# Optimization experiments

Hardware: AMD Instinct MI355X
Metric: run time of the kernel (lower is better)

The kernel has to match this reference:

```python
import jax, jax.numpy as jnp
import numpy as np

HEADS = 2
NEG_SLOPE = 0.2
B, T, N, F_IN = 4, 8, 10000, 128
HID = 128
E = 320000
OUT = 10


def setup_inputs() -> dict:
    key = jax.random.key(0)
    ks = jax.random.split(key, 16)
    d = {}
    d['x_seq'] = jax.random.normal(ks[0], (B, T, N, F_IN), dtype=jnp.float32)
    d['edge_index'] = jax.random.randint(ks[1], (T, 2, E), 0, N)
    def glorot(k, shape):
        fan = shape[0]
        return jax.random.normal(k, shape, dtype=jnp.float32) / jnp.sqrt(jnp.float32(fan))
    # GAT layer 1: in=F_IN, heads=2, out per head=HID
    d['W1'] = glorot(ks[2], (F_IN, HEADS * HID))
    d['a_src1'] = jax.random.normal(ks[3], (HEADS, HID), dtype=jnp.float32) * 0.1
    d['a_dst1'] = jax.random.normal(ks[4], (HEADS, HID), dtype=jnp.float32) * 0.1
    d['b1'] = jnp.zeros((HEADS * HID,), jnp.float32)
    # GAT layer 2: in=2*HID
    d['W2'] = glorot(ks[5], (HEADS * HID, HEADS * HID))
    d['a_src2'] = jax.random.normal(ks[6], (HEADS, HID), dtype=jnp.float32) * 0.1
    d['a_dst2'] = jax.random.normal(ks[7], (HEADS, HID), dtype=jnp.float32) * 0.1
    d['b2'] = jnp.zeros((HEADS * HID,), jnp.float32)
    # GRU: input 2*HID, hidden HID (torch layout: [3H, in])
    d['Wih'] = glorot(ks[8], (3 * HID, HEADS * HID)) 
    d['Whh'] = glorot(ks[9], (3 * HID, HID))
    d['bih'] = jnp.zeros((3 * HID,), jnp.float32)
    d['bhh'] = jnp.zeros((3 * HID,), jnp.float32)
    # classifier
    d['Wc'] = glorot(ks[10], (HID, OUT))
    d['bc'] = jnp.zeros((OUT,), jnp.float32)
    return d


def _gat_layer(x, src, dst, W, a_s, a_d, b):
    # x: [N, Fin]; src/dst: [E'] (self-loops included)
    n = x.shape[0]
    dh = a_s.shape[1]
    h = (x @ W).reshape(n, HEADS, dh)                    # [N, H, dh]
    es = jnp.einsum('nhd,hd->nh', h, a_s)                # [N, H]
    ed = jnp.einsum('nhd,hd->nh', h, a_d)
    e = jax.nn.leaky_relu(es[src] + ed[dst], NEG_SLOPE)  # [E', H]
    m = jax.ops.segment_max(e, dst, num_segments=n)      # stable softmax per dst
    ex = jnp.exp(e - m[dst])
    denom = jax.ops.segment_sum(ex, dst, num_segments=n)
    alpha = ex / denom[dst]                              # [E', H]
    out = jax.ops.segment_sum(h[src] * alpha[:, :, None], dst, num_segments=n)
    return out.reshape(n, HEADS * dh) + b


def _gru(seq, Wih, Whh, bih, bhh):
    # seq: [B, T, D] -> outputs [B, T, H]
    b, t, _ = seq.shape
    hdim = Whh.shape[1]
    def step(hprev, x):
        gi = x @ Wih.T + bih
        gh = hprev @ Whh.T + bhh
        i_r, i_z, i_n = jnp.split(gi, 3, axis=-1)
        h_r, h_z, h_n = jnp.split(gh, 3, axis=-1)
        r = jax.nn.sigmoid(i_r + h_r)
        z = jax.nn.sigmoid(i_z + h_z)
        nn_ = jnp.tanh(i_n + r * h_n)
        hnew = (1.0 - z) * nn_ + z * hprev
        return hnew, hnew
    h0 = jnp.zeros((b, hdim), seq.dtype)
    _, ys = jax.lax.scan(step, h0, jnp.swapaxes(seq, 0, 1))
    return jnp.swapaxes(ys, 0, 1)


def reference(x_seq, edge_index, W1, a_src1, a_dst1, b1, W2, a_src2, a_dst2, b2,
              Wih, Whh, bih, bhh, Wc, bc):
    n = x_seq.shape[2]
    loops = jnp.arange(n)
    # add self-loops per timestep (PyG GATConv default)
    src = jnp.concatenate([edge_index[:, 0], jnp.broadcast_to(loops, (edge_index.shape[0], n))], axis=1)
    dst = jnp.concatenate([edge_index[:, 1], jnp.broadcast_to(loops, (edge_index.shape[0], n))], axis=1)

    def block(x, s, d):
        x1 = jax.nn.relu(_gat_layer(x, s, d, W1, a_src1, a_dst1, b1))
        x2 = _gat_layer(x1, s, d, W2, a_src2, a_dst2, b2)
        return x2.mean(axis=0)                          # node mean-pool -> [2*HID]

    per_t = jax.vmap(lambda xt, s, d: jax.vmap(lambda xb: block(xb, s, d))(xt))
    # x_seq [B,T,N,F] -> [T,B,N,F]
    pooled = per_t(jnp.swapaxes(x_seq, 0, 1), src, dst)  # [T, B, 2*HID]
    seq = jnp.swapaxes(pooled, 0, 1)                     # [B, T, 2*HID]

    rnn_out = _gru(seq, Wih, Whh, bih, bhh)              # [B, T, HID]
    final = rnn_out.mean(axis=1)                         # dropout p=0 is identity
    return final @ Wc + bc
```

## Files before the change

kernel.cpp:

```cpp
#include <hip/hip_runtime.h>
#include <cstdint>

#define NB 4
#define TT 8
#define NN 10000
#define FIN 128
#define HID 128
#define EE 320000
#define DMODEL 256
#define MTOT (NB*NN)
#define NEG 0.2f

__device__ __forceinline__ float leaky(float x){ return x >= 0.f ? x : NEG*x; }

__global__ void hist_kernel(const int* __restrict__ eidx, int* __restrict__ counts){
  int idx = blockIdx.x*256 + threadIdx.x;
  int t = idx / EE, e = idx - t*EE;
  int dst = eidx[(size_t)t*2*EE + EE + e];
  atomicAdd(&counts[t*NN + dst], 1);
}

__global__ void scan_kernel(const int* __restrict__ counts, int* __restrict__ rp,
                            int* __restrict__ cursor){
  int t = blockIdx.x; int tid = threadIdx.x;
  __shared__ int lds[256];
  const int CH = 40;
  int lo = tid*CH, hi = lo+CH < NN ? lo+CH : NN;
  int s = 0;
  for (int i = lo; i < hi; ++i) s += counts[t*NN + i];
  lds[tid] = s; __syncthreads();
  for (int off = 1; off < 256; off <<= 1){
    int v = (tid >= off) ? lds[tid-off] : 0; __syncthreads();
    lds[tid] += v; __syncthreads();
  }
  int run = (tid == 0) ? 0 : lds[tid-1];
  for (int i = lo; i < hi; ++i){
    rp[t*(NN+1) + i] = run; cursor[t*NN + i] = run; run += counts[t*NN + i];
  }
  if (tid == 255) rp[t*(NN+1) + NN] = lds[255];
}

__global__ void scatter_kernel(const int* __restrict__ eidx, int* __restrict__ cursor,
                               int* __restrict__ ssrc){
  int idx = blockIdx.x*256 + threadIdx.x;
  int t = idx / EE, e = idx - t*EE;
  int src = eidx[(size_t)t*2*EE + e];
  int dst = eidx[(size_t)t*2*EE + EE + e];
  int pos = atomicAdd(&cursor[t*NN + dst], 1);
  ssrc[(size_t)t*EE + pos] = src;
}

template<int K>
__global__ __launch_bounds__(256) void gemm_attn_kernel(const float* __restrict__ A0,
    const float* __restrict__ A1, size_t bstride,
    const float* __restrict__ W, const float* __restrict__ av_s, const float* __restrict__ av_d,
    float* __restrict__ C, float* __restrict__ es, float* __restrict__ ed, int M){
  __shared__ float As[16][132];
  __shared__ float Bs[16][128];
  int tid = threadIdx.x;
  int r0 = blockIdx.x*128, c0 = blockIdx.y*128;
  int ty = tid >> 4, tx = tid & 15;

  int cq = (tid & 3)*4;
  const float* a0r0; const float* a0r1; const float* a1r0 = nullptr; const float* a1r1 = nullptr;
  {
    int r_ = r0 + (tid >> 2); if (r_ >= M) r_ = M-1;
    int b = r_/NN, n = r_ - b*NN;
    a0r0 = A0 + (size_t)b*bstride + (size_t)n*128 + cq;
    if (K > 128) a1r0 = A1 + (size_t)r_*128 + cq;
    r_ = r0 + 64 + (tid >> 2); if (r_ >= M) r_ = M-1;
    b = r_/NN; n = r_ - b*NN;
    a0r1 = A0 + (size_t)b*bstride + (size_t)n*128 + cq;
    if (K > 128) a1r1 = A1 + (size_t)r_*128 + cq;
  }
  const float* brow0 = W + (size_t)(tid>>5)*DMODEL + c0 + (tid & 31)*4;
  const float* brow1 = W + (size_t)((tid>>5)+8)*DMODEL + c0 + (tid & 31)*4;

  float acc[8][8];
  #pragma unroll
  for (int i = 0; i < 8; ++i)
    #pragma unroll
    for (int j = 0; j < 8; ++j) acc[i][j] = 0.f;

  int r_loc = tid >> 2;
  #pragma unroll 1
  for (int half = 0; half < K/128; ++half){
    const float* pr0 = half ? a1r0 : a0r0;
    const float* pr1 = half ? a1r1 : a0r1;
    #pragma unroll 1
    for (int k0 = 0; k0 < 128; k0 += 16){
      int kab = half*128 + k0;
      float4 a0v = *(const float4*)(pr0 + k0);
      float4 a1v = *(const float4*)(pr1 + k0);
      float4 b0v = *(const float4*)(brow0 + (size_t)kab*DMODEL);
      float4 b1v = *(const float4*)(brow1 + (size_t)kab*DMODEL);
      __syncthreads();
      As[cq+0][r_loc] = a0v.x; As[cq+1][r_loc] = a0v.y; As[cq+2][r_loc] = a0v.z; As[cq+3][r_loc] = a0v.w;
      As[cq+0][64+r_loc] = a1v.x; As[cq+1][64+r_loc] = a1v.y; As[cq+2][64+r_loc] = a1v.z; As[cq+3][64+r_loc] = a1v.w;
      *(float4*)&Bs[tid>>5][(tid&31)*4]     = b0v;
      *(float4*)&Bs[(tid>>5)+8][(tid&31)*4] = b1v;
      __syncthreads();
      #pragma unroll
      for (int kk = 0; kk < 16; ++kk){
        float4 aA = *(const float4*)&As[kk][ty*4];
        float4 aB = *(const float4*)&As[kk][64+ty*4];
        float4 bA = *(const float4*)&Bs[kk][tx*4];
        float4 bB = *(const float4*)&Bs[kk][64+tx*4];
        float ar[8] = {aA.x,aA.y,aA.z,aA.w,aB.x,aB.y,aB.z,aB.w};
        float br[8] = {bA.x,bA.y,bA.z,bA.w,bB.x,bB.y,bB.z,bB.w};
        #pragma unroll
        for (int i = 0; i < 8; ++i)
          #pragma unroll
          for (int j = 0; j < 8; ++j) acc[i][j] += ar[i]*br[j];
      }
    }
  }

  float as_c[8], ad_c[8];
  #pragma unroll
  for (int j = 0; j < 8; ++j){
    int c = c0 + (j < 4 ? tx*4+j : 64+tx*4+(j-4));
    as_c[j] = av_s[c]; ad_c[j] = av_d[c];
  }
  int hsel = c0 >> 7;
  float* Ch = C + (size_t)hsel*M*128;
  #pragma unroll
  for (int ii = 0; ii < 8; ++ii){
    int r = r0 + (ii < 4 ? ty*4+ii : 64+ty*4+(ii-4));
    float ls = 0.f, ld_ = 0.f;
    #pragma unroll
    for (int j = 0; j < 8; ++j){ ls += acc[ii][j]*as_c[j]; ld_ += acc[ii][j]*ad_c[j]; }
    #pragma unroll
    for (int o = 8; o > 0; o >>= 1){ ls += __shfl_down(ls, o); ld_ += __shfl_down(ld_, o); }
    if (r < M){
      if (tx == 0){ es[(size_t)hsel*M + r] = ls; ed[(size_t)hsel*M + r] = ld_; }
      *(float4*)&Ch[(size_t)r*128 + tx*4]      = make_float4(acc[ii][0],acc[ii][1],acc[ii][2],acc[ii][3]);
      *(float4*)&Ch[(size_t)r*128 + 64 + tx*4] = make_float4(acc[ii][4],acc[ii][5],acc[ii][6],acc[ii][7]);
    }
  }
}

__global__ __launch_bounds__(128) void agg_kernel(const float* __restrict__ H,
    const float* __restrict__ es, const float* __restrict__ ed,
    const int* __restrict__ rp, const int* __restrict__ ssrc,
    const float* __restrict__ bias, float* __restrict__ out, int do_relu){
  int d = blockIdx.x; int ph = blockIdx.y;
  int h = ph & 1, b = ph >> 1;
  int tid = threadIdx.x;
  const size_t reg = (size_t)h*MTOT + (size_t)b*NN;
  const float* esh = es + reg;
  const float* edh = ed + reg;
  const float* Hh  = H + reg*128;
  int e0 = rp[d], e1 = rp[d+1];
  __shared__ float sred[2];
  __shared__ float sbc2[2];
  __shared__ unsigned int offs[128];
  __shared__ float lal[128];

  float edv  = edh[d];
  float self = leaky(esh[d] + edv);

  float m = self;
  for (int e = e0 + tid; e < e1; e += 128) m = fmaxf(m, leaky(esh[ssrc[e]] + edv));
  #pragma unroll
  for (int o = 32; o > 0; o >>= 1) m = fmaxf(m, __shfl_down(m, o));
  int w = tid >> 6, lane = tid & 63;
  if (lane == 0) sred[w] = m;
  __syncthreads();
  if (tid == 0) sbc2[0] = fmaxf(sred[0], sred[1]);
  __syncthreads();
  m = sbc2[0];

  float s0 = (tid == 0) ? expf(self - m) : 0.f;
  for (int e = e0 + tid; e < e1; e += 128) s0 += expf(leaky(esh[ssrc[e]] + edv) - m);
  #pragma unroll
  for (int o = 32; o > 0; o >>= 1) s0 += __shfl_down(s0, o);
  if (lane == 0) sred[w] = s0;
  __syncthreads();
  if (tid == 0) sbc2[1] = 1.f/(sred[0] + sred[1]);
  __syncthreads();
  float inv = sbc2[1];

  float acc = expf(self - m) * inv * Hh[(size_t)d*128 + tid];
  const char* Hb = (const char*)Hh + (size_t)tid*4;
  for (int ch = e0; ch < e1; ch += 128){
    int nc = (e1 - ch < 128) ? (e1 - ch) : 128;
    __syncthreads();
    if (tid < nc){
      int s = ssrc[ch + tid];
      offs[tid] = (unsigned int)(s*512);
      lal[tid]  = expf(leaky(esh[s] + edv) - m) * inv;
    }
    __syncthreads();
    int i = 0;
    float a0 = 0.f, a1 = 0.f, a2 = 0.f, a3 = 0.f;
    for (; i + 4 <= nc; i += 4){
      a0 += lal[i+0] * *(const float*)(Hb + offs[i+0]);
      a1 += lal[i+1] * *(const float*)(Hb + offs[i+1]);
      a2 += lal[i+2] * *(const float*)(Hb + offs[i+2]);
      a3 += lal[i+3] * *(const float*)(Hb + offs[i+3]);
    }
    for (; i < nc; ++i) a0 += lal[i] * *(const float*)(Hb + offs[i]);
    acc += (a0 + a1) + (a2 + a3);
  }
  acc += bias[h*128 + tid];
  if (do_relu) acc = fmaxf(acc, 0.f);
  out[(reg + d)*128 + tid] = acc;
}

#define PCH 64
__global__ void pool1_kernel(const float* __restrict__ X2, float* __restrict__ part){
  int b = blockIdx.x / PCH; int ch = blockIdx.x % PCH; int c = threadIdx.x;
  const int RPC = (NN + PCH - 1) / PCH;
  int d0 = ch*RPC, d1 = d0+RPC < NN ? d0+RPC : NN;
  int hreg = c >> 7, cw = c & 127;
  const float* Xr = X2 + ((size_t)hreg*MTOT + (size_t)b*NN)*128 + cw;
  float s = 0.f;
  for (int d = d0; d < d1; ++d) s += Xr[(size_t)d*128];
  part[(size_t)blockIdx.x*DMODEL + c] = s;
}
__global__ void pool2_kernel(const float* __restrict__ part, float* __restrict__ pooled, int t){
  int b = blockIdx.x; int c = threadIdx.x;
  float s = 0.f;
  for (int ch = 0; ch < PCH; ++ch) s += part[(size_t)(b*PCH + ch)*DMODEL + c];
  pooled[(size_t)(t*NB + b)*DMODEL + c] = s * (1.f/NN);
}

__global__ __launch_bounds__(384) void gi_kernel(const float* __restrict__ pooled,
    const float* __restrict__ Wih, const float* __restrict__ bih, float* __restrict__ gi){
  int row = blockIdx.x; int j = threadIdx.x;
  __shared__ float xs[256];
  if (j < 256) xs[j] = pooled[(size_t)row*DMODEL + j];
  __syncthreads();
  const float4* Wr = (const float4*)(Wih + (size_t)j*DMODEL);
  float s = bih[j];
  #pragma unroll 8
  for (int k = 0; k < 64; ++k){
    float4 wv = Wr[k];
    s += wv.x*xs[k*4] + wv.y*xs[k*4+1] + wv.z*xs[k*4+2] + wv.w*xs[k*4+3];
  }
  gi[(size_t)row*384 + j] = s;
}

__global__ __launch_bounds__(384) void rec_kernel(const float* __restrict__ gi,
    const float* __restrict__ Whh, const float* __restrict__ bhh,
    const float* __restrict__ Wc, const float* __restrict__ bc, float* __restrict__ outp){
  int b = blockIdx.x; int j = threadIdx.x;
  __shared__ float hs[128], ghs[384], fin[128];
  if (j < 128) hs[j] = 0.f;
  float macc = 0.f;
  const float4* Ur = (const float4*)(Whh + (size_t)j*HID);
  float bh = bhh[j];
  for (int t = 0; t < TT; ++t){
    __syncthreads();
    float s = bh;
    #pragma unroll 8
    for (int k = 0; k < 32; ++k){
      float4 wv = Ur[k];
      s += wv.x*hs[k*4] + wv.y*hs[k*4+1] + wv.z*hs[k*4+2] + wv.w*hs[k*4+3];
    }
    ghs[j] = s; __syncthreads();
    float hnew = 0.f;
    if (j < 128){
      const float* g = gi + (size_t)(t*NB + b)*384;
      float r = 1.f/(1.f + expf(-(g[j] + ghs[j])));
      float z = 1.f/(1.f + expf(-(g[128+j] + ghs[128+j])));
      float n = tanhf(g[256+j] + r*ghs[256+j]);
      hnew = (1.f - z)*n + z*hs[j];
    }
    __syncthreads();
    if (j < 128){ hs[j] = hnew; macc += hnew; }
  }
  if (j < 128) fin[j] = macc * (1.f/TT);
  __syncthreads();
  if (j < 10){
    float s = bc[j];
    for (int k = 0; k < 128; ++k) s += fin[k]*Wc[k*10 + j];
    outp[b*10 + j] = s;
  }
}

extern "C" void kernel_launch(void* const* d_in, const int* in_sizes, int n_in,
                              void* d_out, int out_size, void* d_ws, size_t ws_size,
                              hipStream_t stream){
  const float* x_seq = (const float*)d_in[0];
  const int*   eidx  = (const int*)d_in[1];
  const float* W1    = (const float*)d_in[2];
  const float* a_s1  = (const float*)d_in[3];
  const float* a_d1  = (const float*)d_in[4];
  const float* b1    = (const float*)d_in[5];
  const float* W2    = (const float*)d_in[6];
  const float* a_s2  = (const float*)d_in[7];
  const float* a_d2  = (const float*)d_in[8];
  const float* b2    = (const float*)d_in[9];
  const float* Wih   = (const float*)d_in[10];
  const float* Whh   = (const float*)d_in[11];
  const float* bih   = (const float*)d_in[12];
  const float* bhh   = (const float*)d_in[13];
  const float* Wc    = (const float*)d_in[14];
  const float* bc    = (const float*)d_in[15];
  float* outp = (float*)d_out;

  char* ws = (char*)d_ws;
  size_t off = 0;
  auto alloc = [&](size_t bytes)->char*{
    char* p = ws + off; off += (bytes + 511) & ~(size_t)511; return p;
  };
  int*   counts = (int*)  alloc((size_t)TT*NN*4);
  int*   rp     = (int*)  alloc((size_t)TT*(NN+1)*4);
  int*   cursor = (int*)  alloc((size_t)TT*NN*4);
  int*   ssrc   = (int*)  alloc((size_t)TT*EE*4);
  float* H      = (float*)alloc((size_t)MTOT*DMODEL*4);
  float* X1     = (float*)alloc((size_t)MTOT*DMODEL*4);
  float* es     = (float*)alloc((size_t)2*MTOT*4);
  float* ed     = (float*)alloc((size_t)2*MTOT*4);
  float* part   = (float*)alloc((size_t)NB*PCH*DMODEL*4);
  float* pooled = (float*)alloc((size_t)TT*NB*DMODEL*4);
  float* gib    = (float*)alloc((size_t)TT*NB*384*4);
  (void)ws_size; (void)in_sizes; (void)n_in; (void)out_size;

  const int M = MTOT;
  const int GX = (M + 127)/128;

  hipMemsetAsync(counts, 0, (size_t)TT*NN*4, stream);
  hist_kernel   <<<(TT*EE)/256, 256, 0, stream>>>(eidx, counts);
  scan_kernel   <<<TT, 256, 0, stream>>>(counts, rp, cursor);
  scatter_kernel<<<(TT*EE)/256, 256, 0, stream>>>(eidx, cursor, ssrc);

  for (int t = 0; t < TT; ++t){
    const int* rpt = rp + t*(NN+1);
    const int* st  = ssrc + (size_t)t*EE;
    gemm_attn_kernel<FIN><<<dim3(GX, 2), 256, 0, stream>>>(
        x_seq + (size_t)t*NN*FIN, nullptr, (size_t)TT*NN*FIN, W1, a_s1, a_d1, H, es, ed, M);
    agg_kernel<<<dim3(NN, NB*2), 128, 0, stream>>>(H, es, ed, rpt, st, b1, X1, 1);
    gemm_attn_kernel<DMODEL><<<dim3(GX, 2), 256, 0, stream>>>(
        X1, X1 + (size_t)M*128, (size_t)NN*128, W2, a_s2, a_d2, H, es, ed, M);
    agg_kernel<<<dim3(NN, NB*2), 128, 0, stream>>>(H, es, ed, rpt, st, b2, X1, 0);
    pool1_kernel<<<NB*PCH, 256, 0, stream>>>(X1, part);
    pool2_kernel<<<NB, 256, 0, stream>>>(part, pooled, t);
  }
  gi_kernel <<<TT*NB, 384, 0, stream>>>(pooled, Wih, bih, gib);
  rec_kernel<<<NB, 384, 0, stream>>>(gib, Whh, bhh, Wc, bc, outp);
}
```

Baseline: 4.213 ms.

## Use online softmax in GAT aggregation and interleave batch/head blocks per node

Result: faster. 3.894 ms (-7.6%).

```diff
diff --git a/kernel.cpp b/kernel.cpp
--- a/kernel.cpp
+++ b/kernel.cpp
@@ -144,7 +144,9 @@
     const float* __restrict__ es, const float* __restrict__ ed,
     const int* __restrict__ rp, const int* __restrict__ ssrc,
     const float* __restrict__ bias, float* __restrict__ out, int do_relu){
-  int d = blockIdx.x; int ph = blockIdx.y;
+  int bid = blockIdx.x;
+  int ph = bid & 7;
+  int d  = bid >> 3;
   int h = ph & 1, b = ph >> 1;
   int tid = threadIdx.x;
   const size_t reg = (size_t)h*MTOT + (size_t)b*NN;
@@ -152,33 +154,43 @@
   const float* edh = ed + reg;
   const float* Hh  = H + reg*128;
   int e0 = rp[d], e1 = rp[d+1];
-  __shared__ float sred[2];
+  __shared__ float smm[2], sss[2];
   __shared__ float sbc2[2];
+  __shared__ float vcache[128];
   __shared__ unsigned int offs[128];
   __shared__ float lal[128];
 
   float edv  = edh[d];
   float self = leaky(esh[d] + edv);
 
-  float m = self;
-  for (int e = e0 + tid; e < e1; e += 128) m = fmaxf(m, leaky(esh[ssrc[e]] + edv));
+  float m = -1e30f, ssum = 0.f;
+  for (int e = e0 + tid; e < e1; e += 128){
+    int s = ssrc[e];
+    float v = leaky(esh[s] + edv);
+    if (e - e0 < 128){ vcache[tid] = v; offs[tid] = (unsigned int)(s*512); }
+    float mn = fmaxf(m, v);
+    ssum = ssum*expf(m - mn) + expf(v - mn);
+    m = mn;
+  }
   #pragma unroll
-  for (int o = 32; o > 0; o >>= 1) m = fmaxf(m, __shfl_down(m, o));
+  for (int o = 32; o > 0; o >>= 1){
+    float m2 = __shfl_down(m, o);
+    float s2 = __shfl_down(ssum, o);
+    float mn = fmaxf(m, m2);
+    ssum = ssum*expf(m - mn) + s2*expf(m2 - mn);
+    m = mn;
+  }
   int w = tid >> 6, lane = tid & 63;
-  if (lane == 0) sred[w] = m;
+  if (lane == 0){ smm[w] = m; sss[w] = ssum; }
   __syncthreads();
-  if (tid == 0) sbc2[0] = fmaxf(sred[0], sred[1]);
+  if (tid == 0){
+    float mA = smm[0], sA = sss[0], mB = smm[1], sB = sss[1];
+    float mn = fmaxf(fmaxf(mA, mB), self);
+    float st = sA*expf(mA - mn) + sB*expf(mB - mn) + expf(self - mn);
+    sbc2[0] = mn; sbc2[1] = 1.f/st;
+  }
   __syncthreads();
   m = sbc2[0];
-
-  float s0 = (tid == 0) ? expf(self - m) : 0.f;
-  for (int e = e0 + tid; e < e1; e += 128) s0 += expf(leaky(esh[ssrc[e]] + edv) - m);
-  #pragma unroll
-  for (int o = 32; o > 0; o >>= 1) s0 += __shfl_down(s0, o);
-  if (lane == 0) sred[w] = s0;
-  __syncthreads();
-  if (tid == 0) sbc2[1] = 1.f/(sred[0] + sred[1]);
-  __syncthreads();
   float inv = sbc2[1];
 
   float acc = expf(self - m) * inv * Hh[(size_t)d*128 + tid];
@@ -187,9 +199,13 @@
     int nc = (e1 - ch < 128) ? (e1 - ch) : 128;
     __syncthreads();
     if (tid < nc){
-      int s = ssrc[ch + tid];
-      offs[tid] = (unsigned int)(s*512);
-      lal[tid]  = expf(leaky(esh[s] + edv) - m) * inv;
+      if (ch == e0){
+        lal[tid] = expf(vcache[tid] - m) * inv;
+      } else {
+        int s = ssrc[ch + tid];
+        offs[tid] = (unsigned int)(s*512);
+        lal[tid]  = expf(leaky(esh[s] + edv) - m) * inv;
+      }
     }
     __syncthreads();
     int i = 0;
@@ -332,10 +348,10 @@
     const int* st  = ssrc + (size_t)t*EE;
     gemm_attn_kernel<FIN><<<dim3(GX, 2), 256, 0, stream>>>(
         x_seq + (size_t)t*NN*FIN, nullptr, (size_t)TT*NN*FIN, W1, a_s1, a_d1, H, es, ed, M);
-    agg_kernel<<<dim3(NN, NB*2), 128, 0, stream>>>(H, es, ed, rpt, st, b1, X1, 1);
+    agg_kernel<<<8*NN, 128, 0, stream>>>(H, es, ed, rpt, st, b1, X1, 1);
     gemm_attn_kernel<DMODEL><<<dim3(GX, 2), 256, 0, stream>>>(
         X1, X1 + (size_t)M*128, (size_t)NN*128, W2, a_s2, a_d2, H, es, ed, M);
-    agg_kernel<<<dim3(NN, NB*2), 128, 0, stream>>>(H, es, ed, rpt, st, b2, X1, 0);
+    agg_kernel<<<8*NN, 128, 0, stream>>>(H, es, ed, rpt, st, b2, X1, 0);
     pool1_kernel<<<NB*PCH, 256, 0, stream>>>(X1, part);
     pool2_kernel<<<NB, 256, 0, stream>>>(part, pooled, t);
   }
```

## Restructure GAT aggregation: cache first-chunk logits, float4 gathers, interleave batch/head blocks

Applied to the files above, without the earlier changes.

Measured after the change: 3.393 ms. 19.5% less time.

```diff
diff --git a/kernel.cpp b/kernel.cpp
--- a/kernel.cpp
+++ b/kernel.cpp
@@ -144,7 +144,9 @@
     const float* __restrict__ es, const float* __restrict__ ed,
     const int* __restrict__ rp, const int* __restrict__ ssrc,
     const float* __restrict__ bias, float* __restrict__ out, int do_relu){
-  int d = blockIdx.x; int ph = blockIdx.y;
+  int bid = blockIdx.x;
+  int ph = bid & 7;
+  int d  = bid >> 3;
   int h = ph & 1, b = ph >> 1;
   int tid = threadIdx.x;
   const size_t reg = (size_t)h*MTOT + (size_t)b*NN;
@@ -152,60 +154,99 @@
   const float* edh = ed + reg;
   const float* Hh  = H + reg*128;
   int e0 = rp[d], e1 = rp[d+1];
+  int deg = e1 - e0;
+  int nc0 = deg < 128 ? deg : 128;
   __shared__ float sred[2];
   __shared__ float sbc2[2];
-  __shared__ unsigned int offs[128];
-  __shared__ float lal[128];
+  __shared__ float vcache[128];
+  __shared__ unsigned int offsc[128];
+  __shared__ float2 lalf2[128];
+  __shared__ float4 sacc[128];
 
   float edv  = edh[d];
   float self = leaky(esh[d] + edv);
+  int w = tid >> 6, lane = tid & 63;
 
   float m = self;
-  for (int e = e0 + tid; e < e1; e += 128) m = fmaxf(m, leaky(esh[ssrc[e]] + edv));
+  for (int e = e0 + tid; e < e1; e += 128){
+    int s = ssrc[e];
+    float v = leaky(esh[s] + edv);
+    if (e - e0 < 128){ vcache[tid] = v; offsc[tid] = (unsigned int)(s*512); }
+    m = fmaxf(m, v);
+  }
   #pragma unroll
   for (int o = 32; o > 0; o >>= 1) m = fmaxf(m, __shfl_down(m, o));
-  int w = tid >> 6, lane = tid & 63;
   if (lane == 0) sred[w] = m;
   __syncthreads();
   if (tid == 0) sbc2[0] = fmaxf(sred[0], sred[1]);
   __syncthreads();
   m = sbc2[0];
 
-  float s0 = (tid == 0) ? expf(self - m) : 0.f;
-  for (int e = e0 + tid; e < e1; e += 128) s0 += expf(leaky(esh[ssrc[e]] + edv) - m);
-  #pragma unroll
-  for (int o = 32; o > 0; o >>= 1) s0 += __shfl_down(s0, o);
-  if (lane == 0) sred[w] = s0;
-  __syncthreads();
-  if (tid == 0) sbc2[1] = 1.f/(sred[0] + sred[1]);
+  float p = 0.f;
+  if (tid < nc0) p = expf(vcache[tid] - m);
+  float ssum = p;
+  for (int e = e0 + 128 + tid; e < e1; e += 128)
+    ssum += expf(leaky(esh[ssrc[e]] + edv) - m);
+  #pragma unroll
+  for (int o = 32; o > 0; o >>= 1) ssum += __shfl_down(ssum, o);
+  if (lane == 0) sred[w] = ssum;
+  __syncthreads();
+  if (tid == 0) sbc2[1] = 1.f/(sred[0] + sred[1] + expf(self - m));
   __syncthreads();
   float inv = sbc2[1];
-
-  float acc = expf(self - m) * inv * Hh[(size_t)d*128 + tid];
-  const char* Hb = (const char*)Hh + (size_t)tid*4;
+  if (tid < nc0) lalf2[tid] = make_float2(p*inv, __uint_as_float(offsc[tid]));
+  __syncthreads();
+
+  int q = tid >> 5, c = tid & 31;
+  const char* Hbase = (const char*)Hh;
+  unsigned cb = (unsigned)(c*16);
+  float4 accA = make_float4(0.f,0.f,0.f,0.f);
+  float4 accB = make_float4(0.f,0.f,0.f,0.f);
   for (int ch = e0; ch < e1; ch += 128){
     int nc = (e1 - ch < 128) ? (e1 - ch) : 128;
-    __syncthreads();
-    if (tid < nc){
-      int s = ssrc[ch + tid];
-      offs[tid] = (unsigned int)(s*512);
-      lal[tid]  = expf(leaky(esh[s] + edv) - m) * inv;
-    }
-    __syncthreads();
-    int i = 0;
-    float a0 = 0.f, a1 = 0.f, a2 = 0.f, a3 = 0.f;
-    for (; i + 4 <= nc; i += 4){
-      a0 += lal[i+0] * *(const float*)(Hb + offs[i+0]);
-      a1 += lal[i+1] * *(const float*)(Hb + offs[i+1]);
-      a2 += lal[i+2] * *(const float*)(Hb + offs[i+2]);
-      a3 += lal[i+3] * *(const float*)(Hb + offs[i+3]);
-    }
-    for (; i < nc; ++i) a0 += lal[i] * *(const float*)(Hb + offs[i]);
-    acc += (a0 + a1) + (a2 + a3);
-  }
-  acc += bias[h*128 + tid];
-  if (do_relu) acc = fmaxf(acc, 0.f);
-  out[(reg + d)*128 + tid] = acc;
+    if (ch > e0){
+      __syncthreads();
+      if (tid < nc){
+        int s = ssrc[ch + tid];
+        lalf2[tid] = make_float2(expf(leaky(esh[s] + edv) - m)*inv,
+                                 __uint_as_float((unsigned int)(s*512)));
+      }
+      __syncthreads();
+    }
+    int i = q;
+    for (; i + 4 < nc; i += 8){
+      float2 l0 = lalf2[i];
+      float2 l1 = lalf2[i+4];
+      float4 h0 = *(const float4*)(Hbase + (__float_as_uint(l0.y) + cb));
+      float4 h1 = *(const float4*)(Hbase + (__float_as_uint(l1.y) + cb));
+      accA.x += l0.x*h0.x; accA.y += l0.x*h0.y; accA.z += l0.x*h0.z; accA.w += l0.x*h0.w;
+      accB.x += l1.x*h1.x; accB.y += l1.x*h1.y; accB.z += l1.x*h1.z; accB.w += l1.x*h1.w;
+    }
+    if (i < nc){
+      float2 l0 = lalf2[i];
+      float4 h0 = *(const float4*)(Hbase + (__float_as_uint(l0.y) + cb));
+      accA.x += l0.x*h0.x; accA.y += l0.x*h0.y; accA.z += l0.x*h0.z; accA.w += l0.x*h0.w;
+    }
+  }
+  accA.x += accB.x; accA.y += accB.y; accA.z += accB.z; accA.w += accB.w;
+  __syncthreads();
+  sacc[tid] = accA;
+  __syncthreads();
+  if (tid < 32){
+    float4 r0 = sacc[tid], r1 = sacc[tid+32], r2 = sacc[tid+64], r3 = sacc[tid+96];
+    float4 r = make_float4(r0.x+r1.x+r2.x+r3.x, r0.y+r1.y+r2.y+r3.y,
+                           r0.z+r1.z+r2.z+r3.z, r0.w+r1.w+r2.w+r3.w);
+    float sw = expf(self - m)*inv;
+    float4 hd = *(const float4*)(Hbase + (size_t)d*512 + tid*16);
+    float4 bv = *(const float4*)(bias + h*128 + tid*4);
+    r.x += sw*hd.x + bv.x; r.y += sw*hd.y + bv.y;
+    r.z += sw*hd.z + bv.z; r.w += sw*hd.w + bv.w;
+    if (do_relu){
+      r.x = fmaxf(r.x, 0.f); r.y = fmaxf(r.y, 0.f);
+      r.z = fmaxf(r.z, 0.f); r.w = fmaxf(r.w, 0.f);
+    }
+    *(float4*)&out[(reg + d)*128 + tid*4] = r;
+  }
 }
 
 #define PCH 64
@@ -332,10 +373,10 @@
     const int* st  = ssrc + (size_t)t*EE;
     gemm_attn_kernel<FIN><<<dim3(GX, 2), 256, 0, stream>>>(
         x_seq + (size_t)t*NN*FIN, nullptr, (size_t)TT*NN*FIN, W1, a_s1, a_d1, H, es, ed, M);
-    agg_kernel<<<dim3(NN, NB*2), 128, 0, stream>>>(H, es, ed, rpt, st, b1, X1, 1);
+    agg_kernel<<<8*NN, 128, 0, stream>>>(H, es, ed, rpt, st, b1, X1, 1);
     gemm_attn_kernel<DMODEL><<<dim3(GX, 2), 256, 0, stream>>>(
         X1, X1 + (size_t)M*128, (size_t)NN*128, W2, a_s2, a_d2, H, es, ed, M);
-    agg_kernel<<<dim3(NN, NB*2), 128, 0, stream>>>(H, es, ed, rpt, st, b2, X1, 0);
+    agg_kernel<<<8*NN, 128, 0, stream>>>(H, es, ed, rpt, st, b2, X1, 0);
     pool1_kernel<<<NB*PCH, 256, 0, stream>>>(X1, part);
     pool2_kernel<<<NB, 256, 0, stream>>>(part, pooled, t);
   }
```
